# Performance work log

Measured on AMD Instinct MI355X. Metric: run time of the kernel, lower is better.

The kernel has to match this reference:

```python
import jax, jax.numpy as jnp
import numpy as np

B, S, D, H = 4, 2048, 512, 8
HD = D // H
POOL_HEADS = 8


def setup_inputs() -> dict:
    key = jax.random.key(0)
    ks = iter(jax.random.split(key, 32))
    p = {}
    p['x'] = jax.random.normal(next(ks), (B, S, D), dtype=jnp.float32)
    p['mask'] = jnp.zeros((B, S), dtype=jnp.float32)  # key_padding_mask (1.0 = padded)
    s = 1.0 / np.sqrt(D)
    for layer in ('1', '2'):
        for name in ('q', 'k', 'v', 'o'):
            p[f'{name}{layer}_w'] = jax.random.normal(next(ks), (D, D), dtype=jnp.float32) * s
            p[f'{name}{layer}_b'] = jnp.zeros((D,), dtype=jnp.float32)
    p['ln1_g'] = jnp.ones((D,), jnp.float32); p['ln1_b'] = jnp.zeros((D,), jnp.float32)
    p['ffn_w1'] = jax.random.normal(next(ks), (D, D), dtype=jnp.float32) * s
    p['ffn_b1'] = jnp.zeros((D,), jnp.float32)
    p['ffn_w2'] = jax.random.normal(next(ks), (D, D), dtype=jnp.float32) * s
    p['ffn_b2'] = jnp.zeros((D,), jnp.float32)
    p['ln2_g'] = jnp.ones((D,), jnp.float32); p['ln2_b'] = jnp.zeros((D,), jnp.float32)
    p['pool_w'] = jax.random.normal(next(ks), (D, POOL_HEADS), dtype=jnp.float32) * s
    p['pool_b'] = jnp.zeros((POOL_HEADS,), jnp.float32)
    return p


def _layernorm(x, g, b, eps=1e-5):
    mu = jnp.mean(x, axis=-1, keepdims=True)
    var = jnp.var(x, axis=-1, keepdims=True)
    return (x - mu) * jax.lax.rsqrt(var + eps) * g + b


def _mha(x, mask, qw, qb, kw, kb, vw, vb, ow, ob):
    b, s, d = x.shape
    q = (x @ qw + qb).reshape(b, s, H, HD)
    k = (x @ kw + kb).reshape(b, s, H, HD)
    v = (x @ vw + vb).reshape(b, s, H, HD)
    scores = jnp.einsum('bihd,bjhd->bhij', q, k) / jnp.sqrt(jnp.float32(HD))
    scores = scores - mask[:, None, None, :] * 1e30  # key_padding_mask
    w = jax.nn.softmax(scores, axis=-1)  # dropout is identity at eval
    out = jnp.einsum('bhij,bjhd->bihd', w, v).reshape(b, s, d)
    return out @ ow + ob


def _pool(x, mask, pw, pb):
    alpha = jax.nn.leaky_relu(x @ pw + pb)            # [B,S,POOL_HEADS]
    alpha = alpha + mask[:, :, None] * -1e16
    alpha = jax.nn.softmax(alpha, axis=1)             # softmax over sequence
    # sum over heads of alpha_h * x, then sum over sequence
    return jnp.einsum('bs,bsd->bd', alpha.sum(axis=-1), x)


def reference(x, mask,
              q1_w, q1_b, k1_w, k1_b, v1_w, v1_b, o1_w, o1_b,
              q2_w, q2_b, k2_w, k2_b, v2_w, v2_b, o2_w, o2_b,
              ln1_g, ln1_b, ffn_w1, ffn_b1, ffn_w2, ffn_b2,
              ln2_g, ln2_b, pool_w, pool_b):
    # F.normalize(x, p=2, dim=-1)
    x = x / jnp.maximum(jnp.linalg.norm(x, axis=-1, keepdims=True), 1e-12)
    h = _mha(x, mask, q1_w, q1_b, k1_w, k1_b, v1_w, v1_b, o1_w, o1_b)
    h = _layernorm(h, ln1_g, ln1_b)
    h = jax.nn.relu(h @ ffn_w1 + ffn_b1) @ ffn_w2 + ffn_b2
    h = _mha(h, mask, q2_w, q2_b, k2_w, k2_b, v2_w, v2_b, o2_w, o2_b)
    h = _layernorm(h, ln2_g, ln2_b)
    return _pool(h, mask, pool_w, pool_b)  # [B, D] patch_feature (cls=False -> logit is None)
```

## Files before the change

kernel.cpp:

```cpp
#include <hip/hip_runtime.h>
#include <hip/hip_bf16.h>
#include <stdint.h>

#define DEVI __device__ __forceinline__

typedef float f32x4 __attribute__((ext_vector_type(4)));
typedef float f32x16 __attribute__((ext_vector_type(16)));
typedef short bf16x8 __attribute__((ext_vector_type(8)));

typedef __attribute__((address_space(3))) unsigned int as3_u32;
typedef __attribute__((address_space(1))) unsigned int as1_u32;

DEVI void gload16(const void* g, void* l) {
  __builtin_amdgcn_global_load_lds((const as1_u32*)g, (as3_u32*)l, 16, 0, 0);
}

DEVI unsigned short bf16r(float f) {
  union { float f; unsigned int u; } v; v.f = f;
  unsigned int u = v.u;
  return (unsigned short)((u + 0x7FFFu + ((u >> 16) & 1u)) >> 16);
}

DEVI float bf2f(unsigned short u) {
  unsigned int x = ((unsigned int)u) << 16;
  union { unsigned int u; float f; } v; v.u = x;
  return v.f;
}

DEVI unsigned int pkbf16(float a, float b) {
  __hip_bfloat162 h = __float22bfloat162_rn(make_float2(a, b));
  return *(unsigned int*)&h;
}

struct PrepArgs {
  const float* w[10];
  const float* b1[3];
  const float* b2[3];
};

__global__ __launch_bounds__(256) void prep_kernel(PrepArgs pa, unsigned short* wt,
                                                   float* qb1, float* qb2) {
  __shared__ float lt[64][65];
  const int slot = blockIdx.z;
  const int n0 = blockIdx.x * 64, k0 = blockIdx.y * 64;
  const float* W = pa.w[slot];
  for (int it = 0; it < 16; it++) {
    int idx = it * 256 + threadIdx.x;
    int kr = idx >> 6, nc = idx & 63;
    lt[kr][nc] = W[(long)(k0 + kr) * 512 + n0 + nc];
  }
  __syncthreads();
  unsigned short* dst = wt + (long)slot * 512 * 512;
  for (int it = 0; it < 16; it++) {
    int idx = it * 256 + threadIdx.x;
    int nr = idx >> 6, kc = idx & 63;
    dst[(long)(n0 + nr) * 512 + k0 + kc] = bf16r(lt[kc][nr]);
  }
  if (blockIdx.x == 0 && blockIdx.y == 0) {
    if (slot < 3) {
      for (int i = threadIdx.x; i < 512; i += 256) qb1[slot * 512 + i] = pa.b1[slot][i];
    } else if (slot >= 6 && slot < 9) {
      for (int i = threadIdx.x; i < 512; i += 256) qb2[(slot - 6) * 512 + i] = pa.b2[slot - 6][i];
    }
  }
}

__global__ __launch_bounds__(256) void l2norm_kernel(const float* __restrict__ x,
                                                     unsigned short* __restrict__ xn) {
  const long row = blockIdx.x;
  const float* xr = x + row * 512;
  float v0 = xr[threadIdx.x], v1 = xr[threadIdx.x + 256];
  float ss = v0 * v0 + v1 * v1;
  #pragma unroll
  for (int off = 32; off > 0; off >>= 1) ss += __shfl_down(ss, off, 64);
  __shared__ float red[4];
  __shared__ float sc[1];
  int w = threadIdx.x >> 6, ln = threadIdx.x & 63;
  if (ln == 0) red[w] = ss;
  __syncthreads();
  if (threadIdx.x == 0) {
    float S = red[0] + red[1] + red[2] + red[3];
    sc[0] = 1.0f / fmaxf(sqrtf(S), 1e-12f);
  }
  __syncthreads();
  float s = sc[0];
  xn[row * 512 + threadIdx.x] = bf16r(v0 * s);
  xn[row * 512 + threadIdx.x + 256] = bf16r(v1 * s);
}

template <int EPI>
__global__ __launch_bounds__(256) void gemm_bt(const unsigned short* __restrict__ A,
                                               const unsigned short* __restrict__ Bt,
                                               const float* __restrict__ bias,
                                               void* __restrict__ Cv, int K, int N,
                                               unsigned short* __restrict__ vtout) {
  __shared__ unsigned short ldsA[128 * 64];
  __shared__ unsigned short ldsB[128 * 64];
  const int tid = threadIdx.x, w = tid >> 6, ln = tid & 63;
  const int bm = blockIdx.x, bn = blockIdx.y;
  const int wm = (w >> 1) * 64, wn = (w & 1) * 64;
  const f32x4 zf = {0.f, 0.f, 0.f, 0.f};
  f32x4 acc[4][4];
  #pragma unroll
  for (int i = 0; i < 4; i++)
    #pragma unroll
    for (int j = 0; j < 4; j++) acc[i][j] = zf;
  const int r8 = ln >> 3, s8 = ln & 7;
  for (int kt = 0; kt < K; kt += 64) {
    #pragma unroll
    for (int i = 0; i < 4; i++) {
      int row = w * 32 + i * 8 + r8;
      gload16(A + (long)(bm * 128 + row) * K + kt + s8 * 8, &ldsA[(w * 32 + i * 8) * 64]);
      gload16(Bt + (long)(bn * 128 + row) * K + kt + s8 * 8, &ldsB[(w * 32 + i * 8) * 64]);
    }
    __syncthreads();
    #pragma unroll
    for (int kk = 0; kk < 2; kk++) {
      bf16x8 af[4], bfr[4];
      #pragma unroll
      for (int mf = 0; mf < 4; mf++) {
        int row = wm + mf * 16 + (ln & 15);
        af[mf] = *(const bf16x8*)&ldsA[row * 64 + kk * 32 + (ln >> 4) * 8];
      }
      #pragma unroll
      for (int nf = 0; nf < 4; nf++) {
        int row = wn + nf * 16 + (ln & 15);
        bfr[nf] = *(const bf16x8*)&ldsB[row * 64 + kk * 32 + (ln >> 4) * 8];
      }
      #pragma unroll
      for (int mf = 0; mf < 4; mf++)
        #pragma unroll
        for (int nf = 0; nf < 4; nf++)
          acc[mf][nf] = __builtin_amdgcn_mfma_f32_16x16x32_bf16(af[mf], bfr[nf], acc[mf][nf], 0, 0, 0);
    }
    __syncthreads();
  }
  const int g = ln >> 4, c = ln & 15;
  #pragma unroll
  for (int mf = 0; mf < 4; mf++) {
    #pragma unroll
    for (int nf = 0; nf < 4; nf++) {
      int col = bn * 128 + wn + nf * 16 + c;
      float bv = bias[col];
      if (EPI == 3 && col >= 1024) {
        long row0 = bm * 128 + wm + mf * 16 + g * 4;
        int b = (int)(row0 >> 11), s = (int)(row0 & 2047);
        int vc = col - 1024, h = vc >> 6, hd = vc & 63;
        ushort4 o;
        o.x = bf16r(acc[mf][nf][0] + bv);
        o.y = bf16r(acc[mf][nf][1] + bv);
        o.z = bf16r(acc[mf][nf][2] + bv);
        o.w = bf16r(acc[mf][nf][3] + bv);
        *(ushort4*)(vtout + ((long)((b * 8 + h) * 64 + hd)) * 2048 + s) = o;
      } else {
        #pragma unroll
        for (int j = 0; j < 4; j++) {
          long row = bm * 128 + wm + mf * 16 + g * 4 + j;
          float v = acc[mf][nf][j] + bv;
          if (EPI == 2) v = v > 0.f ? v : 0.f;
          if (EPI == 0)
            ((float*)Cv)[row * N + col] = v;
          else
            ((unsigned short*)Cv)[row * N + col] = bf16r(v);
        }
      }
    }
  }
}

template <int EPI>
__global__ __launch_bounds__(256) void gemm_bt64(const unsigned short* __restrict__ A,
                                                 const unsigned short* __restrict__ Bt,
                                                 const float* __restrict__ bias,
                                                 void* __restrict__ Cv, int K, int N) {
  __shared__ unsigned short ldsA[128 * 64];
  __shared__ unsigned short ldsB[64 * 64];
  const int tid = threadIdx.x, w = tid >> 6, ln = tid & 63;
  const int bm = blockIdx.x, bn = blockIdx.y;
  const int wm = (w >> 1) * 64, wn = (w & 1) * 32;
  const f32x4 zf = {0.f, 0.f, 0.f, 0.f};
  f32x4 acc[4][2];
  #pragma unroll
  for (int i = 0; i < 4; i++)
    #pragma unroll
    for (int j = 0; j < 2; j++) acc[i][j] = zf;
  const int r8 = ln >> 3, s8 = ln & 7;
  for (int kt = 0; kt < K; kt += 64) {
    #pragma unroll
    for (int i = 0; i < 6; i++) {
      int jj = w * 6 + i;
      if (jj < 16) {
        gload16(A + (long)(bm * 128 + jj * 8 + r8) * K + kt + s8 * 8, &ldsA[jj * 512]);
      } else {
        int jb = jj - 16;
        gload16(Bt + (long)(bn * 64 + jb * 8 + r8) * K + kt + s8 * 8, &ldsB[jb * 512]);
      }
    }
    __syncthreads();
    #pragma unroll
    for (int kk = 0; kk < 2; kk++) {
      bf16x8 af[4], bfr[2];
      #pragma unroll
      for (int mf = 0; mf < 4; mf++)
        af[mf] = *(const bf16x8*)&ldsA[(wm + mf * 16 + (ln & 15)) * 64 + kk * 32 + (ln >> 4) * 8];
      #pragma unroll
      for (int nf = 0; nf < 2; nf++)
        bfr[nf] = *(const bf16x8*)&ldsB[(wn + nf * 16 + (ln & 15)) * 64 + kk * 32 + (ln >> 4) * 8];
      #pragma unroll
      for (int mf = 0; mf < 4; mf++)
        #pragma unroll
        for (int nf = 0; nf < 2; nf++)
          acc[mf][nf] = __builtin_amdgcn_mfma_f32_16x16x32_bf16(af[mf], bfr[nf], acc[mf][nf], 0, 0, 0);
    }
    __syncthreads();
  }
  const int g = ln >> 4, c = ln & 15;
  #pragma unroll
  for (int mf = 0; mf < 4; mf++) {
    #pragma unroll
    for (int nf = 0; nf < 2; nf++) {
      int col = bn * 64 + wn + nf * 16 + c;
      float bv = bias[col];
      #pragma unroll
      for (int j = 0; j < 4; j++) {
        long row = bm * 128 + wm + mf * 16 + g * 4 + j;
        float v = acc[mf][nf][j] + bv;
        if (EPI == 2) v = v > 0.f ? v : 0.f;
        if (EPI == 0)
          ((float*)Cv)[row * N + col] = v;
        else
          ((unsigned short*)Cv)[row * N + col] = bf16r(v);
      }
    }
  }
}

__global__ __launch_bounds__(256, 4) void attn_split_kernel(
    const unsigned short* __restrict__ qkv,
    const unsigned short* __restrict__ vt,
    const float* __restrict__ mask,
    unsigned short* __restrict__ opart,
    float* __restrict__ lpart) {
  const int tid = threadIdx.x, w = tid >> 6, ln = tid & 63;
  const int lo = ln & 31, hi = ln >> 5;
  const int bid = blockIdx.x + 16 * blockIdx.y + 512 * blockIdx.z;
  const int swz = (bid & 7) * 256 + (bid >> 3);
  const int qb = swz & 15, bh = (swz >> 4) & 31, sp = swz >> 9;
  const int b = bh >> 3, h = bh & 7;
  const int q0 = qb * 128 + w * 32;
  const unsigned short* qp = qkv + (long)(b * 2048) * 1536 + h * 64;
  const unsigned short* kp = qp + 512;
  const unsigned short* vtp = vt + (long)bh * 64 * 2048;
  const float* mp = mask + b * 2048;
  const int kt0 = sp * 512;

  __shared__ unsigned short sbuf[2][4096];
  __shared__ float mbuf[512];
  __shared__ int mflag;

  {
    float mv0 = mp[kt0 + tid], mv1 = mp[kt0 + 256 + tid];
    mbuf[tid] = mv0;
    mbuf[tid + 256] = mv1;
    if (tid == 0) mflag = 0;
    __syncthreads();
    if (mv0 != 0.f || mv1 != 0.f) mflag = 1;
    __syncthreads();
  }
  const bool anymask = (mflag != 0);

  const int jj0 = w * 2;
  const char *src0, *src1;
  long step;
  if (w < 2) {
    int r0 = jj0 * 8 + (ln >> 3), r1 = r0 + 8, s = ln & 7;
    src0 = (const char*)kp + 2L * ((long)(kt0 + r0) * 1536 + ((s ^ (r0 & 7)) * 8));
    src1 = (const char*)kp + 2L * ((long)(kt0 + r1) * 1536 + ((s ^ (r1 & 7)) * 8));
    step = 32L * 1536 * 2;
  } else {
    int j0 = (w - 2) * 2;
    int r0 = j0 * 16 + (ln >> 2), r1 = r0 + 16, s = ln & 3;
    src0 = (const char*)vtp + 2L * ((long)r0 * 2048 + kt0 + ((s ^ ((r0 >> 1) & 3)) * 8));
    src1 = (const char*)vtp + 2L * ((long)r1 * 2048 + kt0 + ((s ^ ((r1 >> 1) & 3)) * 8));
    step = 64;
  }
  unsigned short* const d0a = &sbuf[0][jj0 * 512];
  unsigned short* const d0b = d0a + 512;
  unsigned short* const d1a = &sbuf[1][jj0 * 512];
  unsigned short* const d1b = d1a + 512;

  int koffe[4];
  #pragma unroll
  for (int t = 0; t < 4; t++)
    koffe[t] = lo * 64 + (((t * 2 + hi) ^ (lo & 7)) * 8);
  int voffe[4];
  #pragma unroll
  for (int stt = 0; stt < 2; stt++)
    #pragma unroll
    for (int tau = 0; tau < 2; tau++) {
      int vr = tau * 32 + lo;
      voffe[stt * 2 + tau] = 2048 + vr * 32 + ((((stt * 2 + hi) ^ ((vr >> 1) & 3))) * 8);
    }

  bf16x8 qf[4];
  #pragma unroll
  for (int t = 0; t < 4; t++)
    qf[t] = *(const bf16x8*)(qp + (long)(q0 + lo) * 1536 + t * 16 + hi * 8);

  f32x16 oacc[2];
  #pragma unroll
  for (int t = 0; t < 2; t++)
    #pragma unroll
    for (int r = 0; r < 16; r++) oacc[t][r] = 0.f;
  float lsum = 0.f;
  const f32x16 zf16 = oacc[0];
  const float SC = 0.18033688011112042f;

  gload16(src0, d0a);
  gload16(src1, d0b);
  src0 += step; src1 += step;

#define ATTN_BODY(CURB, DA, DB, ITOFF, STAGE_NEXT)                              \
  {                                                                             \
    if (STAGE_NEXT) {                                                           \
      gload16(src0, DA);                                                        \
      gload16(src1, DB);                                                        \
      src0 += step; src1 += step;                                               \
      asm volatile("s_waitcnt vmcnt(2)" ::: "memory");                          \
    } else {                                                                    \
      asm volatile("s_waitcnt vmcnt(0)" ::: "memory");                          \
    }                                                                           \
    __builtin_amdgcn_s_barrier();                                               \
    __builtin_amdgcn_sched_barrier(0);                                          \
    f32x16 sacc = zf16;                                                         \
    _Pragma("unroll")                                                           \
    for (int t = 0; t < 4; t++) {                                               \
      bf16x8 kf = *(const bf16x8*)&sbuf[CURB][koffe[t]];                        \
      sacc = __builtin_amdgcn_mfma_f32_32x32x16_bf16(kf, qf[t], sacc, 0, 0, 0); \
    }                                                                           \
    float e[16];                                                                \
    _Pragma("unroll")                                                           \
    for (int r = 0; r < 16; r++) e[r] = sacc[r] * SC;                           \
    if (anymask) {                                                              \
      float mval = mbuf[(ITOFF) + lo];                                          \
      _Pragma("unroll")                                                         \
      for (int r = 0; r < 16; r++)                                              \
        e[r] -= 1.4426950408889634e30f *                                        \
                __shfl(mval, (r & 3) + 8 * (r >> 2) + 4 * hi, 64);              \
    }                                                                           \
    _Pragma("unroll")                                                           \
    for (int r = 0; r < 16; r++) e[r] = __builtin_amdgcn_exp2f(e[r]);           \
    _Pragma("unroll")                                                           \
    for (int r = 0; r < 16; r++) lsum += e[r];                                  \
    unsigned int cv[8];                                                         \
    _Pragma("unroll")                                                           \
    for (int i = 0; i < 8; i++) cv[i] = pkbf16(e[2 * i], e[2 * i + 1]);         \
    _Pragma("unroll")                                                           \
    for (int stt = 0; stt < 2; stt++) {                                         \
      unsigned int pf[4];                                                       \
      {                                                                         \
        auto r0_ = __builtin_amdgcn_permlane32_swap(cv[stt * 4 + 0],            \
                                                    cv[stt * 4 + 2], false, false); \
        auto r1_ = __builtin_amdgcn_permlane32_swap(cv[stt * 4 + 1],            \
                                                    cv[stt * 4 + 3], false, false); \
        pf[0] = r0_[0]; pf[1] = r1_[0]; pf[2] = r0_[1]; pf[3] = r1_[1];         \
      }                                                                         \
      bf16x8 pfr = *(const bf16x8*)pf;                                          \
      _Pragma("unroll")                                                         \
      for (int tau = 0; tau < 2; tau++) {                                       \
        bf16x8 vf = *(const bf16x8*)&sbuf[CURB][voffe[stt * 2 + tau]];          \
        oacc[tau] = __builtin_amdgcn_mfma_f32_32x32x16_bf16(vf, pfr, oacc[tau], 0, 0, 0); \
      }                                                                         \
    }                                                                           \
    __builtin_amdgcn_sched_barrier(0);                                          \
    __builtin_amdgcn_s_barrier();                                               \
  }

  for (int it2 = 0; it2 < 8; it2++) {
    ATTN_BODY(0, d1a, d1b, it2 * 64, 1)
    ATTN_BODY(1, d0a, d0b, it2 * 64 + 32, (it2 < 7))
  }
#undef ATTN_BODY

  lsum += __shfl_xor(lsum, 32, 64);
  unsigned short* ob = opart + (long)(sp * 32 + bh) * 2048 * 64;
  const long row = q0 + lo;
  #pragma unroll
  for (int tau = 0; tau < 2; tau++) {
    #pragma unroll
    for (int j = 0; j < 4; j++) {
      ushort4 o;
      o.x = bf16r(oacc[tau][4 * j + 0]);
      o.y = bf16r(oacc[tau][4 * j + 1]);
      o.z = bf16r(oacc[tau][4 * j + 2]);
      o.w = bf16r(oacc[tau][4 * j + 3]);
      *(ushort4*)(ob + row * 64 + tau * 32 + j * 8 + hi * 4) = o;
    }
  }
  if (hi == 0)
    lpart[(long)(sp * 32 + bh) * 2048 + row] = lsum;
}

__global__ __launch_bounds__(256) void attn_combine(const unsigned short* __restrict__ opart,
                                                    const float* __restrict__ lpart,
                                                    unsigned short* __restrict__ ao) {
  const long row = blockIdx.x;
  const int b = (int)(row >> 11), q = (int)(row & 2047);
  #pragma unroll
  for (int half = 0; half < 2; half++) {
    int col = threadIdx.x + half * 256;
    int h = col >> 6, hd = col & 63;
    int bh = b * 8 + h;
    float l = 0.f, v = 0.f;
    #pragma unroll
    for (int sp = 0; sp < 4; sp++) {
      l += lpart[(long)(sp * 32 + bh) * 2048 + q];
      v += bf2f(opart[((long)(sp * 32 + bh) * 2048 + q) * 64 + hd]);
    }
    ao[row * 512 + col] = bf16r(v / l);
  }
}

template <int OUTF>
__global__ __launch_bounds__(256) void ln_kernel(const float* __restrict__ in,
                                                 const float* __restrict__ gam,
                                                 const float* __restrict__ bet,
                                                 void* __restrict__ out) {
  const long row = blockIdx.x;
  const float* x = in + row * 512;
  float v0 = x[threadIdx.x], v1 = x[threadIdx.x + 256];
  float s = v0 + v1, ss = v0 * v0 + v1 * v1;
  #pragma unroll
  for (int off = 32; off > 0; off >>= 1) {
    s += __shfl_down(s, off, 64);
    ss += __shfl_down(ss, off, 64);
  }
  __shared__ float red[8];
  __shared__ float mv[2];
  int w = threadIdx.x >> 6, ln = threadIdx.x & 63;
  if (ln == 0) { red[w] = s; red[w + 4] = ss; }
  __syncthreads();
  if (threadIdx.x == 0) {
    float S = red[0] + red[1] + red[2] + red[3];
    float SS = red[4] + red[5] + red[6] + red[7];
    float mu = S * (1.f / 512.f);
    float var = SS * (1.f / 512.f) - mu * mu;
    mv[0] = mu;
    mv[1] = rsqrtf(var + 1e-5f);
  }
  __syncthreads();
  float mu = mv[0], rs = mv[1];
  float o0 = (v0 - mu) * rs * gam[threadIdx.x] + bet[threadIdx.x];
  float o1 = (v1 - mu) * rs * gam[threadIdx.x + 256] + bet[threadIdx.x + 256];
  if (OUTF == 0) {
    ((unsigned short*)out)[row * 512 + threadIdx.x] = bf16r(o0);
    ((unsigned short*)out)[row * 512 + threadIdx.x + 256] = bf16r(o1);
  } else {
    ((float*)out)[row * 512 + threadIdx.x] = o0;
    ((float*)out)[row * 512 + threadIdx.x + 256] = o1;
  }
}

__global__ __launch_bounds__(256) void alpha_kernel(const float* __restrict__ h,
                                                    const float* __restrict__ pw,
                                                    const float* __restrict__ pbias,
                                                    const float* __restrict__ mask,
                                                    float* __restrict__ alpha) {
  int w = threadIdx.x >> 6, ln = threadIdx.x & 63;
  long row = (long)blockIdx.x * 4 + w;
  float p[8];
  #pragma unroll
  for (int k = 0; k < 8; k++) p[k] = 0.f;
  #pragma unroll
  for (int it = 0; it < 8; it++) {
    int d = it * 64 + ln;
    float xv = h[row * 512 + d];
    const float* wr = pw + d * 8;
    #pragma unroll
    for (int k = 0; k < 8; k++) p[k] += xv * wr[k];
  }
  #pragma unroll
  for (int off = 32; off > 0; off >>= 1)
    #pragma unroll
    for (int k = 0; k < 8; k++) p[k] += __shfl_down(p[k], off, 64);
  if (ln == 0) {
    float mterm = mask[row] * (-1e16f);
    #pragma unroll
    for (int k = 0; k < 8; k++) {
      float a = p[k] + pbias[k];
      a = a < 0.f ? 0.01f * a : a;
      alpha[row * 8 + k] = a + mterm;
    }
  }
}

__global__ __launch_bounds__(256) void stats_kernel(const float* __restrict__ alpha,
                                                    float* __restrict__ stats) {
  int b = blockIdx.x >> 3, ph = blockIdx.x & 7;
  const float* a = alpha + (long)b * 2048 * 8 + ph;
  __shared__ float rr[4];
  __shared__ float mm[1];
  int w = threadIdx.x >> 6, ln = threadIdx.x & 63;
  float m = -1e38f;
  for (int s = threadIdx.x; s < 2048; s += 256) m = fmaxf(m, a[(long)s * 8]);
  #pragma unroll
  for (int off = 32; off > 0; off >>= 1) m = fmaxf(m, __shfl_down(m, off, 64));
  if (ln == 0) rr[w] = m;
  __syncthreads();
  if (threadIdx.x == 0) mm[0] = fmaxf(fmaxf(rr[0], rr[1]), fmaxf(rr[2], rr[3]));
  __syncthreads();
  float M = mm[0];
  float sum = 0.f;
  for (int s = threadIdx.x; s < 2048; s += 256) sum += __expf(a[(long)s * 8] - M);
  #pragma unroll
  for (int off = 32; off > 0; off >>= 1) sum += __shfl_down(sum, off, 64);
  __syncthreads();
  if (ln == 0) rr[w] = sum;
  __syncthreads();
  if (threadIdx.x == 0) {
    stats[blockIdx.x * 2] = M;
    stats[blockIdx.x * 2 + 1] = rr[0] + rr[1] + rr[2] + rr[3];
  }
}

__global__ __launch_bounds__(256) void pool_kernel(const float* __restrict__ h,
                                                   const float* __restrict__ alpha,
                                                   const float* __restrict__ stats,
                                                   float* __restrict__ partial) {
  int b = blockIdx.x >> 3, sc = blockIdx.x & 7;
  int s0 = sc * 256;
  __shared__ float wb[256];
  {
    long s = s0 + threadIdx.x;
    const float* a = alpha + ((long)b * 2048 + s) * 8;
    float wsum = 0.f;
    #pragma unroll
    for (int ph = 0; ph < 8; ph++) {
      float M = stats[(b * 8 + ph) * 2], Sm = stats[(b * 8 + ph) * 2 + 1];
      wsum += __expf(a[ph] - M) / Sm;
    }
    wb[threadIdx.x] = wsum;
  }
  __syncthreads();
  float a0 = 0.f, a1 = 0.f;
  const float* hb = h + ((long)b * 2048 + s0) * 512;
  for (int i = 0; i < 256; i++) {
    float wv = wb[i];
    a0 += wv * hb[(long)i * 512 + threadIdx.x];
    a1 += wv * hb[(long)i * 512 + threadIdx.x + 256];
  }
  partial[(long)blockIdx.x * 512 + threadIdx.x] = a0;
  partial[(long)blockIdx.x * 512 + threadIdx.x + 256] = a1;
}

__global__ __launch_bounds__(256) void pool_final(const float* __restrict__ partial,
                                                  float* __restrict__ out) {
  int b = blockIdx.x;
  float a0 = 0.f, a1 = 0.f;
  #pragma unroll
  for (int sc = 0; sc < 8; sc++) {
    a0 += partial[(long)(b * 8 + sc) * 512 + threadIdx.x];
    a1 += partial[(long)(b * 8 + sc) * 512 + threadIdx.x + 256];
  }
  out[b * 512 + threadIdx.x] = a0;
  out[b * 512 + threadIdx.x + 256] = a1;
}

extern "C" void kernel_launch(void* const* d_in, const int* in_sizes, int n_in,
                              void* d_out, int out_size, void* d_ws, size_t ws_size,
                              hipStream_t stream) {
  (void)in_sizes; (void)n_in; (void)out_size;
  if (ws_size < 92274688UL) return;

  const float* x    = (const float*)d_in[0];
  const float* mask = (const float*)d_in[1];
  const float* q1w = (const float*)d_in[2];  const float* q1b = (const float*)d_in[3];
  const float* k1w = (const float*)d_in[4];  const float* k1b = (const float*)d_in[5];
  const float* v1w = (const float*)d_in[6];  const float* v1b = (const float*)d_in[7];
  const float* o1w = (const float*)d_in[8];  const float* o1b = (const float*)d_in[9];
  const float* q2w = (const float*)d_in[10]; const float* q2b = (const float*)d_in[11];
  const float* k2w = (const float*)d_in[12]; const float* k2b = (const float*)d_in[13];
  const float* v2w = (const float*)d_in[14]; const float* v2b = (const float*)d_in[15];
  const float* o2w = (const float*)d_in[16]; const float* o2b = (const float*)d_in[17];
  const float* ln1g = (const float*)d_in[18]; const float* ln1b = (const float*)d_in[19];
  const float* fw1 = (const float*)d_in[20]; const float* fb1 = (const float*)d_in[21];
  const float* fw2 = (const float*)d_in[22]; const float* fb2 = (const float*)d_in[23];
  const float* ln2g = (const float*)d_in[24]; const float* ln2b = (const float*)d_in[25];
  const float* poolw = (const float*)d_in[26]; const float* poolb = (const float*)d_in[27];

  char* ws = (char*)d_ws;
  unsigned short* Wt  = (unsigned short*)(ws + 0);
  float* qb1          = (float*)(ws + 5242880);
  float* qb2          = (float*)(ws + 5249024);
  float* stats        = (float*)(ws + 5255168);
  float* alpha        = (float*)(ws + 5255424);
  float* partial      = (float*)(ws + 5517568);
  unsigned short* qkv = (unsigned short*)(ws + 8388608);
  unsigned short* vt  = (unsigned short*)(ws + 33554432);
  unsigned short* ao  = (unsigned short*)(ws + 41943040);
  float* t            = (float*)(ws + 50331648);
  unsigned short* xn  = (unsigned short*)(ws + 67108864);
  unsigned short* h1  = (unsigned short*)(ws + 75497472);
  unsigned short* f   = (unsigned short*)(ws + 83886080);
  unsigned short* h2  = xn;
  unsigned short* opart = (unsigned short*)(ws + 50331648);
  float* lpart          = (float*)(ws + 83886080);

  PrepArgs pa;
  pa.w[0] = q1w; pa.w[1] = k1w; pa.w[2] = v1w; pa.w[3] = o1w; pa.w[4] = fw1;
  pa.w[5] = fw2; pa.w[6] = q2w; pa.w[7] = k2w; pa.w[8] = v2w; pa.w[9] = o2w;
  pa.b1[0] = q1b; pa.b1[1] = k1b; pa.b1[2] = v1b;
  pa.b2[0] = q2b; pa.b2[1] = k2b; pa.b2[2] = v2b;

  prep_kernel<<<dim3(8, 8, 10), 256, 0, stream>>>(pa, Wt, qb1, qb2);
  l2norm_kernel<<<8192, 256, 0, stream>>>(x, xn);

  gemm_bt<3><<<dim3(64, 12), 256, 0, stream>>>(xn, Wt, qb1, qkv, 512, 1536, vt);
  attn_split_kernel<<<dim3(16, 32, 4), 256, 0, stream>>>(qkv, vt, mask, opart, lpart);
  attn_combine<<<8192, 256, 0, stream>>>(opart, lpart, ao);
  gemm_bt64<0><<<dim3(64, 8), 256, 0, stream>>>(ao, Wt + 3L * 512 * 512, o1b, t, 512, 512);
  ln_kernel<0><<<8192, 256, 0, stream>>>(t, ln1g, ln1b, h1);
  gemm_bt64<2><<<dim3(64, 8), 256, 0, stream>>>(h1, Wt + 4L * 512 * 512, fb1, f, 512, 512);
  gemm_bt64<1><<<dim3(64, 8), 256, 0, stream>>>(f, Wt + 5L * 512 * 512, fb2, h2, 512, 512);

  gemm_bt<3><<<dim3(64, 12), 256, 0, stream>>>(h2, Wt + 6L * 512 * 512, qb2, qkv, 512, 1536, vt);
  attn_split_kernel<<<dim3(16, 32, 4), 256, 0, stream>>>(qkv, vt, mask, opart, lpart);
  attn_combine<<<8192, 256, 0, stream>>>(opart, lpart, ao);
  gemm_bt64<0><<<dim3(64, 8), 256, 0, stream>>>(ao, Wt + 9L * 512 * 512, o2b, t, 512, 512);
  ln_kernel<1><<<8192, 256, 0, stream>>>(t, ln2g, ln2b, t);

  alpha_kernel<<<2048, 256, 0, stream>>>(t, poolw, poolb, mask, alpha);
  stats_kernel<<<32, 256, 0, stream>>>(alpha, stats);
  pool_kernel<<<32, 256, 0, stream>>>(t, alpha, stats, partial);
  pool_final<<<4, 256, 0, stream>>>(partial, (float*)d_out);
}
```

Baseline: 297.9 us.

## Drop split-K attention with combine pass, fuse LN2 with pool alpha

The attention kernel no longer splits the key sequence four ways. Each block now walks all 2048 keys and normalizes its output in-kernel, writing straight to the attention output buffer. This removes the combine kernel and the partial-output traffic, but the grid shrinks from 2048 to 512 blocks, which may underfill the GPU. Separately, layernorm 2 is fused with the pooling alpha projection so the normalized rows are not re-read from memory.

```diff
diff --git a/kernel.cpp b/kernel.cpp
--- a/kernel.cpp
+++ b/kernel.cpp
@@ -19,12 +19,6 @@
   union { float f; unsigned int u; } v; v.f = f;
   unsigned int u = v.u;
   return (unsigned short)((u + 0x7FFFu + ((u >> 16) & 1u)) >> 16);
-}
-
-DEVI float bf2f(unsigned short u) {
-  unsigned int x = ((unsigned int)u) << 16;
-  union { unsigned int u; float f; } v; v.u = x;
-  return v.f;
 }
 
 DEVI unsigned int pkbf16(float a, float b) {
@@ -235,36 +229,38 @@
   }
 }
 
-__global__ __launch_bounds__(256, 4) void attn_split_kernel(
+__global__ __launch_bounds__(256, 4) void attn_kernel(
     const unsigned short* __restrict__ qkv,
     const unsigned short* __restrict__ vt,
     const float* __restrict__ mask,
-    unsigned short* __restrict__ opart,
-    float* __restrict__ lpart) {
+    unsigned short* __restrict__ ao) {
   const int tid = threadIdx.x, w = tid >> 6, ln = tid & 63;
   const int lo = ln & 31, hi = ln >> 5;
-  const int bid = blockIdx.x + 16 * blockIdx.y + 512 * blockIdx.z;
-  const int swz = (bid & 7) * 256 + (bid >> 3);
-  const int qb = swz & 15, bh = (swz >> 4) & 31, sp = swz >> 9;
+  const int bid = blockIdx.x + 16 * blockIdx.y;
+  const int swz = (bid & 7) * 64 + (bid >> 3);
+  const int qb = swz & 15, bh = swz >> 4;
   const int b = bh >> 3, h = bh & 7;
   const int q0 = qb * 128 + w * 32;
   const unsigned short* qp = qkv + (long)(b * 2048) * 1536 + h * 64;
   const unsigned short* kp = qp + 512;
   const unsigned short* vtp = vt + (long)bh * 64 * 2048;
   const float* mp = mask + b * 2048;
-  const int kt0 = sp * 512;
 
   __shared__ unsigned short sbuf[2][4096];
-  __shared__ float mbuf[512];
+  __shared__ float mbuf[2048];
   __shared__ int mflag;
 
   {
-    float mv0 = mp[kt0 + tid], mv1 = mp[kt0 + 256 + tid];
-    mbuf[tid] = mv0;
-    mbuf[tid + 256] = mv1;
+    float acc = 0.f;
+    #pragma unroll
+    for (int i = 0; i < 8; i++) {
+      float mv = mp[i * 256 + tid];
+      mbuf[i * 256 + tid] = mv;
+      acc += fabsf(mv);
+    }
     if (tid == 0) mflag = 0;
     __syncthreads();
-    if (mv0 != 0.f || mv1 != 0.f) mflag = 1;
+    if (acc != 0.f) mflag = 1;
     __syncthreads();
   }
   const bool anymask = (mflag != 0);
@@ -274,14 +270,14 @@
   long step;
   if (w < 2) {
     int r0 = jj0 * 8 + (ln >> 3), r1 = r0 + 8, s = ln & 7;
-    src0 = (const char*)kp + 2L * ((long)(kt0 + r0) * 1536 + ((s ^ (r0 & 7)) * 8));
-    src1 = (const char*)kp + 2L * ((long)(kt0 + r1) * 1536 + ((s ^ (r1 & 7)) * 8));
+    src0 = (const char*)kp + 2L * ((long)r0 * 1536 + ((s ^ (r0 & 7)) * 8));
+    src1 = (const char*)kp + 2L * ((long)r1 * 1536 + ((s ^ (r1 & 7)) * 8));
     step = 32L * 1536 * 2;
   } else {
     int j0 = (w - 2) * 2;
     int r0 = j0 * 16 + (ln >> 2), r1 = r0 + 16, s = ln & 3;
-    src0 = (const char*)vtp + 2L * ((long)r0 * 2048 + kt0 + ((s ^ ((r0 >> 1) & 3)) * 8));
-    src1 = (const char*)vtp + 2L * ((long)r1 * 2048 + kt0 + ((s ^ ((r1 >> 1) & 3)) * 8));
+    src0 = (const char*)vtp + 2L * ((long)r0 * 2048 + ((s ^ ((r0 >> 1) & 3)) * 8));
+    src1 = (const char*)vtp + 2L * ((long)r1 * 2048 + ((s ^ ((r1 >> 1) & 3)) * 8));
     step = 64;
   }
   unsigned short* const d0a = &sbuf[0][jj0 * 512];
@@ -376,56 +372,33 @@
     __builtin_amdgcn_s_barrier();                                               \
   }
 
-  for (int it2 = 0; it2 < 8; it2++) {
+  for (int it2 = 0; it2 < 32; it2++) {
     ATTN_BODY(0, d1a, d1b, it2 * 64, 1)
-    ATTN_BODY(1, d0a, d0b, it2 * 64 + 32, (it2 < 7))
+    ATTN_BODY(1, d0a, d0b, it2 * 64 + 32, (it2 < 31))
   }
 #undef ATTN_BODY
 
   lsum += __shfl_xor(lsum, 32, 64);
-  unsigned short* ob = opart + (long)(sp * 32 + bh) * 2048 * 64;
-  const long row = q0 + lo;
+  const float inv = 1.f / lsum;
+  unsigned short* ob = ao + ((long)(b * 2048) + q0 + lo) * 512 + h * 64;
   #pragma unroll
   for (int tau = 0; tau < 2; tau++) {
     #pragma unroll
     for (int j = 0; j < 4; j++) {
       ushort4 o;
-      o.x = bf16r(oacc[tau][4 * j + 0]);
-      o.y = bf16r(oacc[tau][4 * j + 1]);
-      o.z = bf16r(oacc[tau][4 * j + 2]);
-      o.w = bf16r(oacc[tau][4 * j + 3]);
-      *(ushort4*)(ob + row * 64 + tau * 32 + j * 8 + hi * 4) = o;
-    }
-  }
-  if (hi == 0)
-    lpart[(long)(sp * 32 + bh) * 2048 + row] = lsum;
-}
-
-__global__ __launch_bounds__(256) void attn_combine(const unsigned short* __restrict__ opart,
-                                                    const float* __restrict__ lpart,
-                                                    unsigned short* __restrict__ ao) {
-  const long row = blockIdx.x;
-  const int b = (int)(row >> 11), q = (int)(row & 2047);
-  #pragma unroll
-  for (int half = 0; half < 2; half++) {
-    int col = threadIdx.x + half * 256;
-    int h = col >> 6, hd = col & 63;
-    int bh = b * 8 + h;
-    float l = 0.f, v = 0.f;
-    #pragma unroll
-    for (int sp = 0; sp < 4; sp++) {
-      l += lpart[(long)(sp * 32 + bh) * 2048 + q];
-      v += bf2f(opart[((long)(sp * 32 + bh) * 2048 + q) * 64 + hd]);
-    }
-    ao[row * 512 + col] = bf16r(v / l);
-  }
-}
-
-template <int OUTF>
+      o.x = bf16r(oacc[tau][4 * j + 0] * inv);
+      o.y = bf16r(oacc[tau][4 * j + 1] * inv);
+      o.z = bf16r(oacc[tau][4 * j + 2] * inv);
+      o.w = bf16r(oacc[tau][4 * j + 3] * inv);
+      *(ushort4*)(ob + tau * 32 + j * 8 + hi * 4) = o;
+    }
+  }
+}
+
 __global__ __launch_bounds__(256) void ln_kernel(const float* __restrict__ in,
                                                  const float* __restrict__ gam,
                                                  const float* __restrict__ bet,
-                                                 void* __restrict__ out) {
+                                                 unsigned short* __restrict__ out) {
   const long row = blockIdx.x;
   const float* x = in + row * 512;
   float v0 = x[threadIdx.x], v1 = x[threadIdx.x + 256];
@@ -452,45 +425,65 @@
   float mu = mv[0], rs = mv[1];
   float o0 = (v0 - mu) * rs * gam[threadIdx.x] + bet[threadIdx.x];
   float o1 = (v1 - mu) * rs * gam[threadIdx.x + 256] + bet[threadIdx.x + 256];
-  if (OUTF == 0) {
-    ((unsigned short*)out)[row * 512 + threadIdx.x] = bf16r(o0);
-    ((unsigned short*)out)[row * 512 + threadIdx.x + 256] = bf16r(o1);
-  } else {
-    ((float*)out)[row * 512 + threadIdx.x] = o0;
-    ((float*)out)[row * 512 + threadIdx.x + 256] = o1;
-  }
-}
-
-__global__ __launch_bounds__(256) void alpha_kernel(const float* __restrict__ h,
-                                                    const float* __restrict__ pw,
-                                                    const float* __restrict__ pbias,
-                                                    const float* __restrict__ mask,
-                                                    float* __restrict__ alpha) {
+  out[row * 512 + threadIdx.x] = bf16r(o0);
+  out[row * 512 + threadIdx.x + 256] = bf16r(o1);
+}
+
+__global__ __launch_bounds__(256) void ln2_alpha_kernel(const float* __restrict__ in,
+                                                        const float* __restrict__ gam,
+                                                        const float* __restrict__ bet,
+                                                        const float* __restrict__ pw,
+                                                        const float* __restrict__ pbias,
+                                                        const float* __restrict__ mask,
+                                                        float* __restrict__ out,
+                                                        float* __restrict__ alpha) {
+  const long row = blockIdx.x;
+  const float* x = in + row * 512;
+  float v0 = x[threadIdx.x], v1 = x[threadIdx.x + 256];
+  float s = v0 + v1, ss = v0 * v0 + v1 * v1;
+  #pragma unroll
+  for (int off = 32; off > 0; off >>= 1) {
+    s += __shfl_down(s, off, 64);
+    ss += __shfl_down(ss, off, 64);
+  }
+  __shared__ float red[8];
+  __shared__ float mv[2];
+  __shared__ float pr[4][8];
   int w = threadIdx.x >> 6, ln = threadIdx.x & 63;
-  long row = (long)blockIdx.x * 4 + w;
+  if (ln == 0) { red[w] = s; red[w + 4] = ss; }
+  __syncthreads();
+  if (threadIdx.x == 0) {
+    float S = red[0] + red[1] + red[2] + red[3];
+    float SS = red[4] + red[5] + red[6] + red[7];
+    float mu = S * (1.f / 512.f);
+    float var = SS * (1.f / 512.f) - mu * mu;
+    mv[0] = mu;
+    mv[1] = rsqrtf(var + 1e-5f);
+  }
+  __syncthreads();
+  float mu = mv[0], rs = mv[1];
+  float o0 = (v0 - mu) * rs * gam[threadIdx.x] + bet[threadIdx.x];
+  float o1 = (v1 - mu) * rs * gam[threadIdx.x + 256] + bet[threadIdx.x + 256];
+  out[row * 512 + threadIdx.x] = o0;
+  out[row * 512 + threadIdx.x + 256] = o1;
   float p[8];
-  #pragma unroll
-  for (int k = 0; k < 8; k++) p[k] = 0.f;
-  #pragma unroll
-  for (int it = 0; it < 8; it++) {
-    int d = it * 64 + ln;
-    float xv = h[row * 512 + d];
-    const float* wr = pw + d * 8;
-    #pragma unroll
-    for (int k = 0; k < 8; k++) p[k] += xv * wr[k];
-  }
+  const float* w0 = pw + threadIdx.x * 8;
+  const float* w1 = pw + (threadIdx.x + 256) * 8;
+  #pragma unroll
+  for (int k = 0; k < 8; k++) p[k] = o0 * w0[k] + o1 * w1[k];
   #pragma unroll
   for (int off = 32; off > 0; off >>= 1)
     #pragma unroll
     for (int k = 0; k < 8; k++) p[k] += __shfl_down(p[k], off, 64);
-  if (ln == 0) {
-    float mterm = mask[row] * (-1e16f);
-    #pragma unroll
-    for (int k = 0; k < 8; k++) {
-      float a = p[k] + pbias[k];
-      a = a < 0.f ? 0.01f * a : a;
-      alpha[row * 8 + k] = a + mterm;
-    }
+  if (ln == 0)
+    #pragma unroll
+    for (int k = 0; k < 8; k++) pr[w][k] = p[k];
+  __syncthreads();
+  if (threadIdx.x < 8) {
+    float a = pr[0][threadIdx.x] + pr[1][threadIdx.x] + pr[2][threadIdx.x] + pr[3][threadIdx.x]
+              + pbias[threadIdx.x];
+    a = a < 0.f ? 0.01f * a : a;
+    alpha[row * 8 + threadIdx.x] = a + mask[row] * (-1e16f);
   }
 }
 
@@ -603,8 +596,6 @@
   unsigned short* h1  = (unsigned short*)(ws + 75497472);
   unsigned short* f   = (unsigned short*)(ws + 83886080);
   unsigned short* h2  = xn;
-  unsigned short* opart = (unsigned short*)(ws + 50331648);
-  float* lpart          = (float*)(ws + 83886080);
 
   PrepArgs pa;
   pa.w[0] = q1w; pa.w[1] = k1w; pa.w[2] = v1w; pa.w[3] = o1w; pa.w[4] = fw1;
@@ -616,20 +607,17 @@
   l2norm_kernel<<<8192, 256, 0, stream>>>(x, xn);
 
   gemm_bt<3><<<dim3(64, 12), 256, 0, stream>>>(xn, Wt, qb1, qkv, 512, 1536, vt);
-  attn_split_kernel<<<dim3(16, 32, 4), 256, 0, stream>>>(qkv, vt, mask, opart, lpart);
-  attn_combine<<<8192, 256, 0, stream>>>(opart, lpart, ao);
+  attn_kernel<<<dim3(16, 32), 256, 0, stream>>>(qkv, vt, mask, ao);
   gemm_bt64<0><<<dim3(64, 8), 256, 0, stream>>>(ao, Wt + 3L * 512 * 512, o1b, t, 512, 512);
-  ln_kernel<0><<<8192, 256, 0, stream>>>(t, ln1g, ln1b, h1);
+  ln_kernel<<<8192, 256, 0, stream>>>(t, ln1g, ln1b, h1);
   gemm_bt64<2><<<dim3(64, 8), 256, 0, stream>>>(h1, Wt + 4L * 512 * 512, fb1, f, 512, 512);
   gemm_bt64<1><<<dim3(64, 8), 256, 0, stream>>>(f, Wt + 5L * 512 * 512, fb2, h2, 512, 512);
 
   gemm_bt<3><<<dim3(64, 12), 256, 0, stream>>>(h2, Wt + 6L * 512 * 512, qb2, qkv, 512, 1536, vt);
-  attn_split_kernel<<<dim3(16, 32, 4), 256, 0, stream>>>(qkv, vt, mask, opart, lpart);
-  attn_combine<<<8192, 256, 0, stream>>>(opart, lpart, ao);
+  attn_kernel<<<dim3(16, 32), 256, 0, stream>>>(qkv, vt, mask, ao);
   gemm_bt64<0><<<dim3(64, 8), 256, 0, stream>>>(ao, Wt + 9L * 512 * 512, o2b, t, 512, 512);
-  ln_kernel<1><<<8192, 256, 0, stream>>>(t, ln2g, ln2b, t);
-
-  alpha_kernel<<<2048, 256, 0, stream>>>(t, poolw, poolb, mask, alpha);
+  ln2_alpha_kernel<<<8192, 256, 0, stream>>>(t, ln2g, ln2b, poolw, poolb, mask, t, alpha);
+
   stats_kernel<<<32, 256, 0, stream>>>(alpha, stats);
   pool_kernel<<<32, 256, 0, stream>>>(t, alpha, stats, partial);
   pool_final<<<4, 256, 0, stream>>>(partial, (float*)d_out);
```

Result: no change. 292.5 us (-1.8%).
